# Optimization experiments

Hardware: AMD Instinct MI355X
Metric: run time of the kernel (lower is better)

The kernel has to match this reference:

```python
import jax, jax.numpy as jnp
import numpy as np

N = 100_000      # nodes
E = 1_600_000    # edges (before self-loops)
IN, OUT, HID = 64, 32, 64
BN_EPS = 1e-5

def _mlp(h, w1, b1, g, beta, w2, b2):
    # PyG MLP (num_layers=2, plain_last=True): Linear -> BatchNorm(train) -> ReLU -> Linear
    h = h @ w1 + b1
    mu = jnp.mean(h, axis=0)
    var = jnp.var(h, axis=0)
    h = (h - mu) * jax.lax.rsqrt(var + BN_EPS) * g + beta
    return jax.nn.relu(h) @ w2 + b2

def setup_inputs() -> dict:
    key = jax.random.key(0)
    ks = jax.random.split(key, 12)
    def rn(k, shape):
        fan_in = shape[0]
        return jax.random.normal(k, shape, jnp.float32) / np.sqrt(fan_in)
    x = jax.random.normal(ks[0], (N, IN), jnp.float32)
    pos = jax.random.normal(ks[1], (N, 3), jnp.float32)
    edge_index = jax.random.randint(ks[2], (2, E), 0, N, jnp.int64)
    return {
        "x": x, "pos": pos, "edge_index": edge_index,
        "w_lin": rn(ks[3], (IN, OUT)), "w_src": rn(ks[4], (IN, OUT)), "w_dst": rn(ks[5], (IN, OUT)),
        "pos_w1": rn(ks[6], (3, HID)), "pos_b1": jnp.zeros((HID,), jnp.float32),
        "pos_g": jnp.ones((HID,), jnp.float32), "pos_beta": jnp.zeros((HID,), jnp.float32),
        "pos_w2": rn(ks[7], (HID, OUT)), "pos_b2": jnp.zeros((OUT,), jnp.float32),
        "att_w1": rn(ks[8], (OUT, HID)), "att_b1": jnp.zeros((HID,), jnp.float32),
        "att_g": jnp.ones((HID,), jnp.float32), "att_beta": jnp.zeros((HID,), jnp.float32),
        "att_w2": rn(ks[9], (HID, OUT)), "att_b2": jnp.zeros((OUT,), jnp.float32),
    }

def reference(x, pos, edge_index, w_lin, w_src, w_dst,
              pos_w1, pos_b1, pos_g, pos_beta, pos_w2, pos_b2,
              att_w1, att_b1, att_g, att_beta, att_w2, att_b2):
    n = x.shape[0]
    # add self-loops (PointTransformerConv default add_self_loops=True)
    loops = jnp.arange(n, dtype=edge_index.dtype)
    src = jnp.concatenate([edge_index[0], loops])  # j (message source)
    dst = jnp.concatenate([edge_index[1], loops])  # i (message target)

    alpha_src = x @ w_src          # [N, OUT]
    alpha_dst = x @ w_dst          # [N, OUT]
    x_val = x @ w_lin              # [N, OUT]

    delta = _mlp(pos[dst] - pos[src], pos_w1, pos_b1, pos_g, pos_beta, pos_w2, pos_b2)  # [E', OUT]
    a = _mlp(alpha_dst[dst] - alpha_src[src] + delta, att_w1, att_b1, att_g, att_beta, att_w2, att_b2)

    # per-destination-node, per-channel softmax over incoming edges
    a_max = jax.ops.segment_max(a, dst, num_segments=n)           # [N, OUT]
    a = jnp.exp(a - a_max[dst])
    denom = jax.ops.segment_sum(a, dst, num_segments=n)           # [N, OUT]
    a = a / (denom[dst] + 1e-16)

    msg = a * (x_val[src] + delta)                                # [E', OUT]
    out = jax.ops.segment_sum(msg, dst, num_segments=n)           # [N, OUT]
    return out
```

## Files before the change

kernel.cpp:

```cpp
#include <hip/hip_runtime.h>

typedef unsigned int uint;
typedef unsigned short ushort;

#define BN_EPS 1e-5f

using bf16x8 = __attribute__((ext_vector_type(8))) short;
using f32x16 = __attribute__((ext_vector_type(16))) float;

union FragU { uint w[4]; bf16x8 v; };

__device__ __forceinline__ uint pk2(float lo, float hi) {
    uint r;
    asm("v_cvt_pk_bf16_f32 %0, %1, %2" : "=v"(r) : "v"(lo), "v"(hi));
    return r;
}
__device__ __forceinline__ float bfu_lo(uint u) { return __uint_as_float(u << 16); }
__device__ __forceinline__ float bfu_hi(uint u) { return __uint_as_float(u & 0xffff0000u); }

__device__ __forceinline__ float upk(const uint* p, int idx) {
    uint u = p[idx >> 1];
    return (idx & 1) ? bfu_hi(u) : bfu_lo(u);
}
__device__ __forceinline__ float upq(const uint2* gq, int r) {
// ... 237 lines not shown
{
    int c = threadIdx.x;
    if (c < 64) {
        float b   = bias ? bias[c] : 0.f;
        float m0  = stats[c] * inv_ep;
        float mu  = m0 + b;
        float eq  = stats[64+c] * inv_ep + 2.f*b*m0 + b*b;
        float var = fmaxf(eq - mu * mu, 0.f);
        float sc  = rsqrtf(var + BN_EPS) * g[c];
        bn[c]      = sc;
        bn[64+c]   = beta[c] - mu * sc;
    }
}

__global__ void k_fold1(const float* __restrict__ pw1, const float* __restrict__ pb1,
                        const float* __restrict__ bn1,
                        float* __restrict__ pw1f, float* __restrict__ pb1f)
{
    int i = threadIdx.x;
    if (i < 192) pw1f[i] = pw1[i] * bn1[i & 63];
    if (i < 64)  pb1f[i] = pb1[i] * bn1[i] + bn1[64 + i];
}

__global__ void k_fold2(const float* __restrict__ aw1, const float* __restrict__ ab1,
                        const float* __restrict__ bn2,
                        float* __restrict__ aw1f, float* __restrict__ ab1f)
{
    int i = blockIdx.x * 256 + threadIdx.x;
    if (i < 2048) aw1f[i] = aw1[i] * bn2[i & 63];
    if (i < 64)   ab1f[i] = ab1[i] * bn2[i] + bn2[64 + i];
}

template<bool SORTED>
__global__ __launch_bounds__(256, 3) void k_delta_stats(
    const int* __restrict__ ei, const int* __restrict__ srcs, const int* __restrict__ dsts,
    const float4* __restrict__ pos4,
    const uint* __restrict__ asx, const uint* __restrict__ aDb,
    const float* __restrict__ pw1f, const float* __restrict__ pb1f,
    const float* __restrict__ pw2, const float* __restrict__ pb2,
    const float* __restrict__ aw1,
    float* __restrict__ partD, int nE, int eTot)
{
    const int lane = threadIdx.x & 63;
    const int col  = lane & 31;
    const int h    = lane >> 5;

    __shared__ float redS[4][64], redQ[4][64];
    {
        int w = threadIdx.x >> 6, c = threadIdx.x & 63;
        redS[w][c] = 0.f; redQ[w][c] = 0.f;
    }

    bool quadOK;
    int q2[4];
    FragU fw_pw2[4];
    FragU fw_aw1[2][2];
    uint pb2p[8];
    {
        int rowv[16];
        get_rowmap(col, rowv);
        quadOK = true;
        #pragma unroll
        for (int g = 0; g < 4; g++)
            quadOK = quadOK && (rowv[4*g+1] == rowv[4*g]+1)
                            && (rowv[4*g+2] == rowv[4*g]+2)
                            && (rowv[4*g+3] == rowv[4*g]+3);
        #pragma unroll
        for (int g = 0; g < 4; g++) q2[g] = rowv[4*g] >> 2;
        #pragma unroll
        for (int kt = 0; kt < 4; kt++)
            #pragma unroll
            for (int jw = 0; jw < 4; jw++) {
                int m = 2*jw;
                int c0 = 16*kt + 8*(m>>2) + 4*h + (m&3);
                fw_pw2[kt].w[jw] = pk2(pw2[c0*32 + col], pw2[(c0+1)*32 + col]);
            }
        #pragma unroll
        for (int mt = 0; mt < 2; mt++)
            #pragma unroll
            for (int kt = 0; kt < 2; kt++)
                #pragma unroll
                for (int jw = 0; jw < 4; jw++) {
                    int u0 = rowv[8*kt + 2*jw], u1 = rowv[8*kt + 2*jw + 1];
                    fw_aw1[mt][kt].w[jw] = pk2(aw1[u0*64 + 32*mt + col],
                                               aw1[u1*64 + 32*mt + col]);
                }
        #pragma unroll
        for (int g = 0; g < 8; g++)
            pb2p[g] = pk2(pb2[rowv[2*g]], pb2[rowv[2*g+1]]);
    }

    float sA[32], qA[32];
    #pragma unroll
    for (int i = 0; i < 32; i++) { sA[i] = 0.f; qA[i] = 0.f; }

    const int nT = (eTot + 31) >> 5;
    const int gw = (blockIdx.x << 2) + (threadIdx.x >> 6);
    const int nW = gridDim.x << 2;

    if (quadOK) {
        for (int t = gw; t < nT; t += nW) {
            int e = t*32 + col;
            bool valid = e < eTot;
            int ec = valid ? e : eTot - 1;
            int src, dst;
            edge_sd<SORTED>(ec, ei, srcs, dsts, nE, src, dst);
            float4 ps = pos4[src], pd = pos4[dst];
            uint2 gs2[4], gd2[4];
            {
                const uint* rs = asx + (size_t)src*32;
                const uint* rd = aDb + (size_t)dst*16;
                #pragma unroll
                for (int g = 0; g < 4; g++) gs2[g] = *(const uint2*)(rs + 2*q2[g]);
                #pragma unroll
                for (int g = 0; g < 4; g++) gd2[g] = *(const uint2*)(rd + 2*q2[g]);
            }
            float p0 = pd.x - ps.x, p1 = pd.y - ps.y, p2 = pd.z - ps.z;

            FragU ft[4];
            #pragma unroll
            for (int kt = 0; kt < 4; kt++)
                #pragma unroll
                for (int mm = 0; mm < 2; mm++) {
                    int cb = 16*kt + 8*mm + 4*h;
                    float4 w0 = *(const float4*)(pw1f +       cb);
                    float4 w1 = *(const float4*)(pw1f + 64  + cb);
                    float4 w2 = *(const float4*)(pw1f + 128 + cb);
                    float4 bb = *(const float4*)(pb1f + cb);
                    float t0 = fmaxf(fmaf(p0,w0.x, fmaf(p1,w1.x, fmaf(p2,w2.x, bb.x))), 0.f);
                    float t1 = fmaxf(fmaf(p0,w0.y, fmaf(p1,w1.y, fmaf(p2,w2.y, bb.y))), 0.f);
                    float t2 = fmaxf(fmaf(p0,w0.z, fmaf(p1,w1.z, fmaf(p2,w2.z, bb.z))), 0.f);
                    float t3 = fmaxf(fmaf(p0,w0.w, fmaf(p1,w1.w, fmaf(p2,w2.w, bb.w))), 0.f);
                    ft[kt].w[2*mm+0] = pk2(t0, t1);
                    ft[kt].w[2*mm+1] = pk2(t2, t3);
                }
            f32x16 adl;
            #pragma unroll
            for (int r = 0; r < 16; r++) adl[r] = upk(pb2p, r);
            #pragma unroll
            for (int kt = 0; kt < 4; kt++)
                adl = __builtin_amdgcn_mfma_f32_32x32x16_bf16(fw_pw2[kt].v, ft[kt].v, adl, 0, 0, 0);

            FragU fu[2];
            #pragma unroll
            for (int kt = 0; kt < 2; kt++)
                #pragma unroll
                for (int jw = 0; jw < 4; jw++) {
                    int r0 = 8*kt + 2*jw;
                    fu[kt].w[jw] = pk2(adl[r0]   + upq(gd2, r0)   - upq(gs2, r0),
                                       adl[r0+1] + upq(gd2, r0+1) - upq(gs2, r0+1));
                }

            f32x16 ah0, ah1;
            #pragma unroll
            for (int r = 0; r < 16; r++) { ah0[r] = 0.f; ah1[r] = 0.f; }
            #pragma unroll
            for (int kt = 0; kt < 2; kt++) {
                ah0 = __builtin_amdgcn_mfma_f32_32x32x16_bf16(fw_aw1[0][kt].v, fu[kt].v, ah0, 0, 0, 0);
                ah1 = __builtin_amdgcn_mfma_f32_32x32x16_bf16(fw_aw1[1][kt].v, fu[kt].v, ah1, 0, 0, 0);
            }
            if (valid) {
                #pragma unroll
                for (int r = 0; r < 16; r++) {
                    sA[r]    += ah0[r];
                    qA[r]     = fmaf(ah0[r], ah0[r], qA[r]);
                    sA[16+r] += ah1[r];
                    qA[16+r]  = fmaf(ah1[r], ah1[r], qA[16+r]);
                }
            }
        }
    } else {
        int rowv[16];
        get_rowmap(col, rowv);
        for (int t = gw; t < nT; t += nW) {
            int e = t*32 + col;
            bool valid = e < eTot;
            int ec = valid ? e : eTot - 1;
            int src, dst;
            edge_sd<SORTED>(ec, ei, srcs, dsts, nE, src, dst);
            float4 pd = pos4[dst], ps = pos4[src];
            float p0 = pd.x - ps.x, p1 = pd.y - ps.y, p2 = pd.z - ps.z;
            FragU ft[4];
            #pragma unroll
            for (int kt = 0; kt < 4; kt++)
                #pragma unroll
                for (int mm = 0; mm < 2; mm++) {
                    int cb = 16*kt + 8*mm + 4*h;
                    float4 w0 = *(const float4*)(pw1f +       cb);
                    float4 w1 = *(const float4*)(pw1f + 64  + cb);
                    float4 w2 = *(const float4*)(pw1f + 128 + cb);
                    float4 bb = *(const float4*)(pb1f + cb);
                    float t0 = fmaxf(fmaf(p0,w0.x, fmaf(p1,w1.x, fmaf(p2,w2.x, bb.x))), 0.f);
                    float t1 = fmaxf(fmaf(p0,w0.y, fmaf(p1,w1.y, fmaf(p2,w2.y, bb.y))), 0.f);
                    float t2 = fmaxf(fmaf(p0,w0.z, fmaf(p1,w1.z, fmaf(p2,w2.z, bb.z))), 0.f);
                    float t3 = fmaxf(fmaf(p0,w0.w, fmaf(p1,w1.w, fmaf(p2,w2.w, bb.w))), 0.f);
                    ft[kt].w[2*mm+0] = pk2(t0, t1);
                    ft[kt].w[2*mm+1] = pk2(t2, t3);
                }
            f32x16 adl;
            #pragma unroll
            for (int r = 0; r < 16; r++) adl[r] = upk(pb2p, r);
            #pragma unroll
            for (int kt = 0; kt < 4; kt++)
                adl = __builtin_amdgcn_mfma_f32_32x32x16_bf16(fw_pw2[kt].v, ft[kt].v, adl, 0, 0, 0);
            const ushort* rs = (const ushort*)(asx + (size_t)src*32);
            const ushort* rd = (const ushort*)(aDb + (size_t)dst*16);
            FragU fu[2];
            #pragma unroll
            for (int kt = 0; kt < 2; kt++)
                #pragma unroll
                for (int jw = 0; jw < 4; jw++) {
                    int r0 = 8*kt + 2*jw;
                    float u0 = adl[r0]   + __uint_as_float(((uint)rd[rowv[r0]])   << 16)
                                         - __uint_as_float(((uint)rs[rowv[r0]])   << 16);
                    float u1 = adl[r0+1] + __uint_as_float(((uint)rd[rowv[r0+1]]) << 16)
                                         - __uint_as_float(((uint)rs[rowv[r0+1]]) << 16);
                    fu[kt].w[jw] = pk2(u0, u1);
                }
            f32x16 ah0, ah1;
            #pragma unroll
            for (int r = 0; r < 16; r++) { ah0[r] = 0.f; ah1[r] = 0.f; }
            #pragma unroll
            for (int kt = 0; kt < 2; kt++) {
                ah0 = __builtin_amdgcn_mfma_f32_32x32x16_bf16(fw_aw1[0][kt].v, fu[kt].v, ah0, 0, 0, 0);
                ah1 = __builtin_amdgcn_mfma_f32_32x32x16_bf16(fw_aw1[1][kt].v, fu[kt].v, ah1, 0, 0, 0);
            }
            if (valid) {
                #pragma unroll
                for (int r = 0; r < 16; r++) {
                    sA[r]    += ah0[r];
                    qA[r]     = fmaf(ah0[r], ah0[r], qA[r]);
                    sA[16+r] += ah1[r];
                    qA[16+r]  = fmaf(ah1[r], ah1[r], qA[16+r]);
                }
            }
        }
    }

    __syncthreads();
    {
        int rv[16];
        get_rowmap(col, rv);
        int w = threadIdx.x >> 6;
        #pragma unroll
        for (int idx = 0; idx < 32; idx++) {
            float vs = sA[idx], vq = qA[idx];
            for (int off = 16; off > 0; off >>= 1) {
                vs += __shfl_xor(vs, off, 64);
                vq += __shfl_xor(vq, off, 64);
            }
            if ((threadIdx.x & 31) == 0) {
                int mt = idx >> 4, r = idx & 15;
                int c = 32*mt + rv[r];
                redS[w][c] = vs;
                redQ[w][c] = vq;
            }
        }
    }
    __syncthreads();
    if (threadIdx.x < 64) {
        int c = threadIdx.x;
        float S = redS[0][c] + redS[1][c] + redS[2][c] + redS[3][c];
        float Q = redQ[0][c] + redQ[1][c] + redQ[2][c] + redQ[3][c];
        partD[(size_t)blockIdx.x*128 + c]      = S;
        partD[(size_t)blockIdx.x*128 + 64 + c] = Q;
    }
}

template<bool SORTED>
__global__ __launch_bounds__(256, 3) void k_att_agg(
    const int* __restrict__ ei, const int* __restrict__ srcs, const int* __restrict__ dsts,
    const float4* __restrict__ pos4,
    const uint* __restrict__ asx, const uint* __restrict__ aDb,
    const float* __restrict__ pw1f, const float* __restrict__ pb1f,
    const float* __restrict__ pw2, const float* __restrict__ pb2,
    const float* __restrict__ aw1f, const float* __restrict__ ab1f,
    const float* __restrict__ aw2, const float* __restrict__ ab2,
    float* __restrict__ denom, float* __restrict__ outp,
    int nE, int eTot)
{
    const int lane = threadIdx.x & 63;
    const int col  = lane & 31;
    const int h    = lane >> 5;

    bool quadOK;
    int q2[4];
    FragU fw_pw2[4], fw_aw2[4];
    FragU fw_aw1[2][2];
    uint pb2p[8], ab2p[8], ab1p[16];
    {
        int rowv[16];
        get_rowmap(col, rowv);
        quadOK = true;
        #pragma unroll
        for (int g = 0; g < 4; g++)
            quadOK = quadOK && (rowv[4*g+1] == rowv[4*g]+1)
                            && (rowv[4*g+2] == rowv[4*g]+2)
                            && (rowv[4*g+3] == rowv[4*g]+3);
        #pragma unroll
        for (int g = 0; g < 4; g++) q2[g] = rowv[4*g] >> 2;
        #pragma unroll
        for (int kt = 0; kt < 4; kt++)
            #pragma unroll
            for (int jw = 0; jw < 4; jw++) {
                int m = 2*jw;
                int c0 = 16*kt + 8*(m>>2) + 4*h + (m&3);
                fw_pw2[kt].w[jw] = pk2(pw2[c0*32 + col], pw2[(c0+1)*32 + col]);
                int o0 = 32*(kt>>1) + rowv[8*(kt&1) + m];
                int o1 = 32*(kt>>1) + rowv[8*(kt&1) + m + 1];
                fw_aw2[kt].w[jw] = pk2(aw2[o0*32 + col], aw2[o1*32 + col]);
            }
        #pragma unroll
        for (int mt = 0; mt < 2; mt++)
            #pragma unroll
            for (int kt = 0; kt < 2; kt++)
                #pragma unroll
                for (int jw = 0; jw < 4; jw++) {
                    int u0 = rowv[8*kt + 2*jw], u1 = rowv[8*kt + 2*jw + 1];
                    fw_aw1[mt][kt].w[jw] = pk2(aw1f[u0*64 + 32*mt + col],
                                               aw1f[u1*64 + 32*mt + col]);
                }
        #pragma unroll
        for (int g = 0; g < 8; g++) {
            pb2p[g] = pk2(pb2[rowv[2*g]], pb2[rowv[2*g+1]]);
            ab2p[g] = pk2(ab2[rowv[2*g]], ab2[rowv[2*g+1]]);
            ab1p[g]     = pk2(ab1f[rowv[2*g]],      ab1f[rowv[2*g+1]]);
            ab1p[8 + g] = pk2(ab1f[32 + rowv[2*g]], ab1f[32 + rowv[2*g+1]]);
        }
    }

    const int nT = (eTot + 31) >> 5;
    const int gw = (blockIdx.x << 2) + (threadIdx.x >> 6);
    const int nW = gridDim.x << 2;

    if (quadOK) {
        for (int t = gw; t < nT; t += nW) {
            int e = t*32 + col;
            bool valid = e < eTot;
            int ec = valid ? e : eTot - 1;
            int src, dst;
            edge_sd<SORTED>(ec, ei, srcs, dsts, nE, src, dst);
            float4 ps = pos4[src], pd = pos4[dst];
            uint2 gs2[4], gx2[4], gd2[4];
            {
                const uint* rs = asx + (size_t)src*32;
                #pragma unroll
                for (int g = 0; g < 4; g++) gs2[g] = *(const uint2*)(rs + 2*q2[g]);
                #pragma unroll
                for (int g = 0; g < 4; g++) gx2[g] = *(const uint2*)(rs + 16 + 2*q2[g]);
                const uint* rd = aDb + (size_t)dst*16;
                #pragma unroll
                for (int g = 0; g < 4; g++) gd2[g] = *(const uint2*)(rd + 2*q2[g]);
            }
            float p0 = pd.x - ps.x, p1 = pd.y - ps.y, p2 = pd.z - ps.z;

            FragU ft[4];
            #pragma unroll
            for (int kt = 0; kt < 4; kt++)
                #pragma unroll
                for (int mm = 0; mm < 2; mm++) {
                    int cb = 16*kt + 8*mm + 4*h;
                    float4 w0 = *(const float4*)(pw1f +       cb);
                    float4 w1 = *(const float4*)(pw1f + 64  + cb);
                    float4 w2 = *(const float4*)(pw1f + 128 + cb);
                    float4 bb = *(const float4*)(pb1f + cb);
                    float t0 = fmaxf(fmaf(p0,w0.x, fmaf(p1,w1.x, fmaf(p2,w2.x, bb.x))), 0.f);
                    float t1 = fmaxf(fmaf(p0,w0.y, fmaf(p1,w1.y, fmaf(p2,w2.y, bb.y))), 0.f);
                    float t2 = fmaxf(fmaf(p0,w0.z, fmaf(p1,w1.z, fmaf(p2,w2.z, bb.z))), 0.f);
                    float t3 = fmaxf(fmaf(p0,w0.w, fmaf(p1,w1.w, fmaf(p2,w2.w, bb.w))), 0.f);
                    ft[kt].w[2*mm+0] = pk2(t0, t1);
                    ft[kt].w[2*mm+1] = pk2(t2, t3);
                }
            f32x16 adl;
            #pragma unroll
            for (int r = 0; r < 16; r++) adl[r] = upk(pb2p, r);
            #pragma unroll
            for (int kt = 0; kt < 4; kt++)
                adl = __builtin_amdgcn_mfma_f32_32x32x16_bf16(fw_pw2[kt].v, ft[kt].v, adl, 0, 0, 0);

            FragU fu[2];
            #pragma unroll
            for (int kt = 0; kt < 2; kt++)
                #pragma unroll
                for (int jw = 0; jw < 4; jw++) {
                    int r0 = 8*kt + 2*jw;
                    fu[kt].w[jw] = pk2(adl[r0]   + upq(gd2, r0)   - upq(gs2, r0),
                                       adl[r0+1] + upq(gd2, r0+1) - upq(gs2, r0+1));
                }

            f32x16 ah0, ah1;
            #pragma unroll
            for (int r = 0; r < 16; r++) { ah0[r] = upk(ab1p, r); ah1[r] = upk(ab1p, 16 + r); }
            #pragma unroll
            for (int kt = 0; kt < 2; kt++) {
                ah0 = __builtin_amdgcn_mfma_f32_32x32x16_bf16(fw_aw1[0][kt].v, fu[kt].v, ah0, 0, 0, 0);
                ah1 = __builtin_amdgcn_mfma_f32_32x32x16_bf16(fw_aw1[1][kt].v, fu[kt].v, ah1, 0, 0, 0);
            }
            FragU fh[4];
            #pragma unroll
            for (int q = 0; q < 4; q++)
                #pragma unroll
                for (int jw = 0; jw < 4; jw++) {
                    int r0 = 8*(q&1) + 2*jw;
                    float x0 = (q < 2) ? ah0[r0]   : ah1[r0];
                    float x1 = (q < 2) ? ah0[r0+1] : ah1[r0+1];
                    fh[q].w[jw] = pk2(fmaxf(x0, 0.f), fmaxf(x1, 0.f));
                }
            f32x16 aa;
            #pragma unroll
            for (int r = 0; r < 16; r++) aa[r] = upk(ab2p, r);
            aa = __builtin_amdgcn_mfma_f32_32x32x16_bf16(fw_aw2[0].v, fh[0].v, aa, 0, 0, 0);
// ... 9 lines not shown
                bool eq2  = (__shfl_down(dst, 2, 32)  == dst) && (lw + 2  < 32);
                bool eq4  = (__shfl_down(dst, 4, 32)  == dst) && (lw + 4  < 32);
                bool eq8  = (__shfl_down(dst, 8, 32)  == dst) && (lw + 8  < 32);
                bool eq16 = (__shfl_down(dst, 16, 32) == dst) && (lw + 16 < 32);
                float* drow = denom + (size_t)dst * 32;
                float* orow = outp  + (size_t)dst * 32;
                #pragma unroll
                for (int r = 0; r < 16; r++) {
                    float ea = __expf(fminf(aa[r], 35.f));
                    float ev = valid ? ea : 0.f;
                    float mv = valid ? ea * (upq(gx2, r) + adl[r]) : 0.f;
                    { float a = __shfl_down(ev,1,32),  b = __shfl_down(mv,1,32);  if (eq1)  { ev += a; mv += b; } }
                    { float a = __shfl_down(ev,2,32),  b = __shfl_down(mv,2,32);  if (eq2)  { ev += a; mv += b; } }
                    { float a = __shfl_down(ev,4,32),  b = __shfl_down(mv,4,32);  if (eq4)  { ev += a; mv += b; } }
                    { float a = __shfl_down(ev,8,32),  b = __shfl_down(mv,8,32);  if (eq8)  { ev += a; mv += b; } }
                    { float a = __shfl_down(ev,16,32), b = __shfl_down(mv,16,32); if (eq16) { ev += a; mv += b; } }
                    if (isHead) {
                        int o = 4*q2[r>>2] + (r&3);
                        unsafeAtomicAdd(drow + o, ev);
                        unsafeAtomicAdd(orow + o, mv);
                    }
                }
            } else if (valid) {
                float* drow = denom + (size_t)dst * 32;
                float* orow = outp  + (size_t)dst * 32;
                #pragma unroll
                for (int r = 0; r < 16; r++) {
                    int o = 4*q2[r>>2] + (r&3);
                    float ea = __expf(fminf(aa[r], 35.f));
                    unsafeAtomicAdd(drow + o, ea);
                    unsafeAtomicAdd(orow + o, ea * (upq(gx2, r) + adl[r]));
                }
            }
        }
    } else {
        int rowv[16];
        get_rowmap(col, rowv);
        for (int t = gw; t < nT; t += nW) {
            int e = t*32 + col;
            bool valid = e < eTot;
            int ec = valid ? e : eTot - 1;
            int src, dst;
            edge_sd<SORTED>(ec, ei, srcs, dsts, nE, src, dst);
            float4 pd = pos4[dst], ps = pos4[src];
            float p0 = pd.x - ps.x, p1 = pd.y - ps.y, p2 = pd.z - ps.z;
            FragU ft[4];
            #pragma unroll
            for (int kt = 0; kt < 4; kt++)
                #pragma unroll
                for (int mm = 0; mm < 2; mm++) {
                    int cb = 16*kt + 8*mm + 4*h;
                    float4 w0 = *(const float4*)(pw1f +       cb);
                    float4 w1 = *(const float4*)(pw1f + 64  + cb);
                    float4 w2 = *(const float4*)(pw1f + 128 + cb);
                    float4 bb = *(const float4*)(pb1f + cb);
                    float t0 = fmaxf(fmaf(p0,w0.x, fmaf(p1,w1.x, fmaf(p2,w2.x, bb.x))), 0.f);
                    float t1 = fmaxf(fmaf(p0,w0.y, fmaf(p1,w1.y, fmaf(p2,w2.y, bb.y))), 0.f);
                    float t2 = fmaxf(fmaf(p0,w0.z, fmaf(p1,w1.z, fmaf(p2,w2.z, bb.z))), 0.f);
                    float t3 = fmaxf(fmaf(p0,w0.w, fmaf(p1,w1.w, fmaf(p2,w2.w, bb.w))), 0.f);
                    ft[kt].w[2*mm+0] = pk2(t0, t1);
                    ft[kt].w[2*mm+1] = pk2(t2, t3);
                }
            f32x16 adl;
            #pragma unroll
            for (int r = 0; r < 16; r++) adl[r] = upk(pb2p, r);
            #pragma unroll
            for (int kt = 0; kt < 4; kt++)
                adl = __builtin_amdgcn_mfma_f32_32x32x16_bf16(fw_pw2[kt].v, ft[kt].v, adl, 0, 0, 0);
            const ushort* rs = (const ushort*)(asx + (size_t)src*32);
            const ushort* rd = (const ushort*)(aDb + (size_t)dst*16);
            FragU fu[2];
            float xg[16];
            #pragma unroll
            for (int r = 0; r < 16; r++)
                xg[r] = __uint_as_float(((uint)rs[32 + rowv[r]]) << 16);
            #pragma unroll
            for (int kt = 0; kt < 2; kt++)
                #pragma unroll
                for (int jw = 0; jw < 4; jw++) {
                    int r0 = 8*kt + 2*jw;
                    float u0 = adl[r0]   + __uint_as_float(((uint)rd[rowv[r0]])   << 16)
                                         - __uint_as_float(((uint)rs[rowv[r0]])   << 16);
                    float u1 = adl[r0+1] + __uint_as_float(((uint)rd[rowv[r0+1]]) << 16)
                                         - __uint_as_float(((uint)rs[rowv[r0+1]]) << 16);
                    fu[kt].w[jw] = pk2(u0, u1);
                }
            f32x16 ah0, ah1;
            #pragma unroll
            for (int r = 0; r < 16; r++) { ah0[r] = upk(ab1p, r); ah1[r] = upk(ab1p, 16 + r); }
            #pragma unroll
            for (int kt = 0; kt < 2; kt++) {
                ah0 = __builtin_amdgcn_mfma_f32_32x32x16_bf16(fw_aw1[0][kt].v, fu[kt].v, ah0, 0, 0, 0);
                ah1 = __builtin_amdgcn_mfma_f32_32x32x16_bf16(fw_aw1[1][kt].v, fu[kt].v, ah1, 0, 0, 0);
            }
            FragU fh[4];
            #pragma unroll
            for (int q = 0; q < 4; q++)
                #pragma unroll
                for (int jw = 0; jw < 4; jw++) {
                    int r0 = 8*(q&1) + 2*jw;
                    float x0 = (q < 2) ? ah0[r0]   : ah1[r0];
                    float x1 = (q < 2) ? ah0[r0+1] : ah1[r0+1];
                    fh[q].w[jw] = pk2(fmaxf(x0, 0.f), fmaxf(x1, 0.f));
                }
            f32x16 aa;
            #pragma unroll
            for (int r = 0; r < 16; r++) aa[r] = upk(ab2p, r);
            aa = __builtin_amdgcn_mfma_f32_32x32x16_bf16(fw_aw2[0].v, fh[0].v, aa, 0, 0, 0);
            aa = __builtin_amdgcn_mfma_f32_32x32x16_bf16(fw_aw2[1].v, fh[1].v, aa, 0, 0, 0);
            aa = __builtin_amdgcn_mfma_f32_32x32x16_bf16(fw_aw2[2].v, fh[2].v, aa, 0, 0, 0);
            aa = __builtin_amdgcn_mfma_f32_32x32x16_bf16(fw_aw2[3].v, fh[3].v, aa, 0, 0, 0);
            if (SORTED) {
                int lw = lane & 31;
                int dprev = __shfl_up(dst, 1, 32);
                bool isHead = (lw == 0) || (dprev != dst);
                bool eq1  = (__shfl_down(dst, 1, 32)  == dst) && (lw + 1  < 32);
                bool eq2  = (__shfl_down(dst, 2, 32)  == dst) && (lw + 2  < 32);
                bool eq4  = (__shfl_down(dst, 4, 32)  == dst) && (lw + 4  < 32);
// ... 63 lines not shown
    const float* ab2   = (const float*)d_in[17];
    float* out = (float*)d_out;

    const int nNodes = in_sizes[0] / 64;
    const int nE     = in_sizes[2] / 2;
    const int eTot   = nE + nNodes;

    const int PMBLK = 1024;
    const int DBLK  = 2048;

    const size_t nF = (size_t)nNodes * 32;
    uint*   asx   = (uint*)d_ws;
    uint*   aDb   = asx + (size_t)nNodes*32;
    float*  pos4  = (float*)(aDb + (size_t)nNodes*16);
    float*  denom = pos4 + (size_t)nNodes*4;
    float*  stats = denom + nF;
    float*  bn1   = stats + 512;
    float*  bn2   = bn1 + 128;
    float*  pw1f  = bn2 + 128;
    float*  pb1f  = pw1f + 192;
    float*  aw1f  = pb1f + 64;
    float*  ab1f  = aw1f + 2048;
    float*  partM = ab1f + 64;
    float*  partD = partM + (size_t)PMBLK*9;
    float*  fend  = partD + (size_t)DBLK*128;

    int* cnt    = (int*)fend;
    int* cur    = cnt + nNodes;
    int* blkS   = cur + nNodes;
    int* blkOff = blkS + 256;
    int* srcs   = blkOff + 256;
    int* dsts   = srcs + eTot;

    size_t need_sorted = ((char*)(dsts + eTot)) - ((char*)d_ws);
    const bool sorted = ws_size >= need_sorted;

    const int nb = (nNodes + SCH - 1) / SCH;

    hipMemsetAsync(out,   0, nF * sizeof(float), stream);
    hipMemsetAsync(denom, 0, nF * sizeof(float), stream);

    k_node_lin<<<(nNodes + 255) / 256, 256, 0, stream>>>(
        x, w_src, w_dst, w_lin, asx, aDb, nNodes);
    k_pos4<<<(nNodes + 255) / 256, 256, 0, stream>>>(pos, (float4*)pos4, nNodes);

    k_pos_mom<<<PMBLK, 256, 0, stream>>>(ei, (const float4*)pos4, partM, nE);
    k_bn1_mom<<<1, 64, 0, stream>>>(partM, PMBLK, pw1, pb1, pg, pbeta, bn1,
                                    1.0f / (float)eTot);
    k_fold1<<<1, 256, 0, stream>>>(pw1, pb1, bn1, pw1f, pb1f);

    if (sorted) {
        hipMemsetAsync(cnt, 0, (size_t)nNodes * sizeof(int), stream);
        k_hist<<<(eTot + 255) / 256, 256, 0, stream>>>(ei, cnt, nE, eTot);
        k_scan1<<<nb, 256, 0, stream>>>(cnt, cur, blkS, nNodes);
        k_scan2<<<1, 256, 0, stream>>>(blkS, blkOff, nb);
        k_scan3<<<nb, 256, 0, stream>>>(cur, blkOff, nNodes);
        k_rank<<<(eTot + 255) / 256, 256, 0, stream>>>(ei, cur, srcs, dsts, nE, eTot);

        k_delta_stats<true><<<DBLK, 256, 0, stream>>>(
            ei, srcs, dsts, (const float4*)pos4, asx, aDb,
            pw1f, pb1f, pw2, pb2, aw1, partD, nE, eTot);
        k_red_stats<<<128, 256, 0, stream>>>(partD, stats + 128, DBLK);
        k_bn_fin<<<1, 64, 0, stream>>>(stats + 128, ag, abeta, ab1, bn2, 1.0f / (float)eTot);
        k_fold2<<<8, 256, 0, stream>>>(aw1, ab1, bn2, aw1f, ab1f);
        k_att_agg<true><<<DBLK, 256, 0, stream>>>(
            ei, srcs, dsts, (const float4*)pos4, asx, aDb,
            pw1f, pb1f, pw2, pb2, aw1f, ab1f, aw2, ab2, denom, out, nE, eTot);
// ... 14 lines not shown
```

Baseline: 930.4 us.

## Stage gathered source rows through swizzled LDS with cooperative 16-byte loads

In both edge kernels, each wave now cooperatively loads the 128-byte source-node rows (alpha_src and x_val) for its 32 edges. Eight lanes share each row and issue contiguous uint4 loads, which are written into a per-wave XOR-swizzled LDS buffer and read back later in the fragment layout the MFMA path needs. This replaces the scattered 8-byte per-lane gathers from global memory with coalesced row loads and moves the readback after the first MFMA to hide latency. It adds 16 KB of LDS per block, and the launch-bounds occupancy hint drops from 3 to 2 blocks. Wave-local LDS reuse across loop iterations depends on lockstep execution within the wave, since no barrier separates them.

Measured after the change: 852.7 us. 1.09x faster.

```diff
diff --git a/kernel.cpp b/kernel.cpp
--- a/kernel.cpp
+++ b/kernel.cpp
@@ -293,7 +293,7 @@
 }
 
 template<bool SORTED>
-__global__ __launch_bounds__(256, 3) void k_delta_stats(
+__global__ __launch_bounds__(256, 2) void k_delta_stats(
     const int* __restrict__ ei, const int* __restrict__ srcs, const int* __restrict__ dsts,
     const float4* __restrict__ pos4,
     const uint* __restrict__ asx, const uint* __restrict__ aDb,
@@ -305,8 +305,10 @@
     const int lane = threadIdx.x & 63;
     const int col  = lane & 31;
     const int h    = lane >> 5;
+    const int wid  = threadIdx.x >> 6;
 
     __shared__ float redS[4][64], redQ[4][64];
+    __shared__ uint sbuf[4][1024];
     {
         int w = threadIdx.x >> 6, c = threadIdx.x & 63;
         redS[w][c] = 0.f; redQ[w][c] = 0.f;
@@ -366,13 +368,18 @@
             int ec = valid ? e : eTot - 1;
             int src, dst;
             edge_sd<SORTED>(ec, ei, srcs, dsts, nE, src, dst);
+            #pragma unroll
+            for (int it = 0; it < 4; it++) {
+                int j  = it*8 + (lane >> 3);
+                int sj = __shfl(src, j, 64);
+                int w  = lane & 7;
+                uint4 v = *(const uint4*)(asx + (size_t)sj*32 + w*4);
+                *(uint4*)&sbuf[wid][j*32 + ((w ^ (j & 7)) << 2)] = v;
+            }
             float4 ps = pos4[src], pd = pos4[dst];
-            uint2 gs2[4], gd2[4];
+            uint2 gd2[4];
             {
-                const uint* rs = asx + (size_t)src*32;
                 const uint* rd = aDb + (size_t)dst*16;
-                #pragma unroll
-                for (int g = 0; g < 4; g++) gs2[g] = *(const uint2*)(rs + 2*q2[g]);
                 #pragma unroll
                 for (int g = 0; g < 4; g++) gd2[g] = *(const uint2*)(rd + 2*q2[g]);
             }
@@ -401,6 +408,13 @@
             #pragma unroll
             for (int kt = 0; kt < 4; kt++)
                 adl = __builtin_amdgcn_mfma_f32_32x32x16_bf16(fw_pw2[kt].v, ft[kt].v, adl, 0, 0, 0);
+
+            uint2 gs2[4];
+            #pragma unroll
+            for (int g = 0; g < 4; g++) {
+                int wq = q2[g] >> 1, hf = (q2[g] & 1) << 1;
+                gs2[g] = *(const uint2*)&sbuf[wid][col*32 + ((wq ^ (col & 7)) << 2) + hf];
+            }
 
             FragU fu[2];
             #pragma unroll
@@ -529,7 +543,7 @@
 }
 
 template<bool SORTED>
-__global__ __launch_bounds__(256, 3) void k_att_agg(
+__global__ __launch_bounds__(256, 2) void k_att_agg(
     const int* __restrict__ ei, const int* __restrict__ srcs, const int* __restrict__ dsts,
     const float4* __restrict__ pos4,
     const uint* __restrict__ asx, const uint* __restrict__ aDb,
@@ -543,6 +557,9 @@
     const int lane = threadIdx.x & 63;
     const int col  = lane & 31;
     const int h    = lane >> 5;
+    const int wid  = threadIdx.x >> 6;
+
+    __shared__ uint sbuf[4][1024];
 
     bool quadOK;
     int q2[4];
@@ -601,14 +618,17 @@
             int ec = valid ? e : eTot - 1;
             int src, dst;
             edge_sd<SORTED>(ec, ei, srcs, dsts, nE, src, dst);
+            #pragma unroll
+            for (int it = 0; it < 4; it++) {
+                int j  = it*8 + (lane >> 3);
+                int sj = __shfl(src, j, 64);
+                int w  = lane & 7;
+                uint4 v = *(const uint4*)(asx + (size_t)sj*32 + w*4);
+                *(uint4*)&sbuf[wid][j*32 + ((w ^ (j & 7)) << 2)] = v;
+            }
             float4 ps = pos4[src], pd = pos4[dst];
-            uint2 gs2[4], gx2[4], gd2[4];
+            uint2 gd2[4];
             {
-                const uint* rs = asx + (size_t)src*32;
-                #pragma unroll
-                for (int g = 0; g < 4; g++) gs2[g] = *(const uint2*)(rs + 2*q2[g]);
-                #pragma unroll
-                for (int g = 0; g < 4; g++) gx2[g] = *(const uint2*)(rs + 16 + 2*q2[g]);
                 const uint* rd = aDb + (size_t)dst*16;
                 #pragma unroll
                 for (int g = 0; g < 4; g++) gd2[g] = *(const uint2*)(rd + 2*q2[g]);
@@ -638,6 +658,14 @@
             #pragma unroll
             for (int kt = 0; kt < 4; kt++)
                 adl = __builtin_amdgcn_mfma_f32_32x32x16_bf16(fw_pw2[kt].v, ft[kt].v, adl, 0, 0, 0);
+
+            uint2 gs2[4], gx2[4];
+            #pragma unroll
+            for (int g = 0; g < 4; g++) {
+                int wq = q2[g] >> 1, hf = (q2[g] & 1) << 1;
+                gs2[g] = *(const uint2*)&sbuf[wid][col*32 + ((wq ^ (col & 7)) << 2) + hf];
+                gx2[g] = *(const uint2*)&sbuf[wid][col*32 + (((4 + wq) ^ (col & 7)) << 2) + hf];
+            }
 
             FragU fu[2];
             #pragma unroll
```

## Software-pipeline source-row gathers through LDS in attention aggregation kernel

Applied to the files above, without the earlier changes.

In k_att_agg the per-edge source feature rows (asx) are now fetched one tile ahead. Each wave issues coalesced 16-byte loads, with source indices broadcast by shuffle, and stages them in a swizzled shared-memory buffer, so gather latency overlaps the current tile's MFMA work and scattered 8-byte loads become wide loads. k_delta_stats merges its quad and non-quad loops into one loop with branches inside. Both kernels drop launch_bounds occupancy from 3 to 2 blocks per CU to leave room for the extra prefetch registers. The cost is more registers and LDS, lower occupancy, and an extra redundant prefetch on the last iteration.

Measured after the change: 812.4 us, median of 2. -12.7%, faster.

```diff
diff --git a/kernel.cpp b/kernel.cpp
--- a/kernel.cpp
+++ b/kernel.cpp
@@ -293,7 +293,7 @@
 }
 
 template<bool SORTED>
-__global__ __launch_bounds__(256, 3) void k_delta_stats(
+__global__ __launch_bounds__(256, 2) void k_delta_stats(
     const int* __restrict__ ei, const int* __restrict__ srcs, const int* __restrict__ dsts,
     const float4* __restrict__ pos4,
     const uint* __restrict__ asx, const uint* __restrict__ aDb,
@@ -317,8 +317,8 @@
     FragU fw_pw2[4];
     FragU fw_aw1[2][2];
     uint pb2p[8];
+    int rowv[16];
     {
-        int rowv[16];
         get_rowmap(col, rowv);
         quadOK = true;
         #pragma unroll
@@ -359,24 +359,242 @@
     const int gw = (blockIdx.x << 2) + (threadIdx.x >> 6);
     const int nW = gridDim.x << 2;
 
+    for (int t = gw; t < nT; t += nW) {
+        int e = t*32 + col;
+        bool valid = e < eTot;
+        int ec = valid ? e : eTot - 1;
+        int src, dst;
+        edge_sd<SORTED>(ec, ei, srcs, dsts, nE, src, dst);
+        float4 ps = pos4[src], pd = pos4[dst];
+        float p0 = pd.x - ps.x, p1 = pd.y - ps.y, p2 = pd.z - ps.z;
+
+        uint2 gs2[4], gd2[4];
+        float gSs[16], gDs[16];
+        if (quadOK) {
+            const uint* rs = asx + (size_t)src*32;
+            const uint* rd = aDb + (size_t)dst*16;
+            #pragma unroll
+            for (int g = 0; g < 4; g++) gs2[g] = *(const uint2*)(rs + 2*q2[g]);
+            #pragma unroll
+            for (int g = 0; g < 4; g++) gd2[g] = *(const uint2*)(rd + 2*q2[g]);
+        } else {
+            const ushort* rs = (const ushort*)(asx + (size_t)src*32);
+            const ushort* rd = (const ushort*)(aDb + (size_t)dst*16);
+            #pragma unroll
+            for (int r = 0; r < 16; r++) {
+                gSs[r] = __uint_as_float(((uint)rs[rowv[r]]) << 16);
+                gDs[r] = __uint_as_float(((uint)rd[rowv[r]]) << 16);
+            }
+        }
+
+        FragU ft[4];
+        #pragma unroll
+        for (int kt = 0; kt < 4; kt++)
+            #pragma unroll
+            for (int mm = 0; mm < 2; mm++) {
+                int cb = 16*kt + 8*mm + 4*h;
+                float4 w0 = *(const float4*)(pw1f +       cb);
+                float4 w1 = *(const float4*)(pw1f + 64  + cb);
+                float4 w2 = *(const float4*)(pw1f + 128 + cb);
+                float4 bb = *(const float4*)(pb1f + cb);
+                float t0 = fmaxf(fmaf(p0,w0.x, fmaf(p1,w1.x, fmaf(p2,w2.x, bb.x))), 0.f);
+                float t1 = fmaxf(fmaf(p0,w0.y, fmaf(p1,w1.y, fmaf(p2,w2.y, bb.y))), 0.f);
+                float t2 = fmaxf(fmaf(p0,w0.z, fmaf(p1,w1.z, fmaf(p2,w2.z, bb.z))), 0.f);
+                float t3 = fmaxf(fmaf(p0,w0.w, fmaf(p1,w1.w, fmaf(p2,w2.w, bb.w))), 0.f);
+                ft[kt].w[2*mm+0] = pk2(t0, t1);
+                ft[kt].w[2*mm+1] = pk2(t2, t3);
+            }
+        f32x16 adl;
+        #pragma unroll
+        for (int r = 0; r < 16; r++) adl[r] = upk(pb2p, r);
+        #pragma unroll
+        for (int kt = 0; kt < 4; kt++)
+            adl = __builtin_amdgcn_mfma_f32_32x32x16_bf16(fw_pw2[kt].v, ft[kt].v, adl, 0, 0, 0);
+
+        FragU fu[2];
+        if (quadOK) {
+            #pragma unroll
+            for (int kt = 0; kt < 2; kt++)
+                #pragma unroll
+                for (int jw = 0; jw < 4; jw++) {
+                    int r0 = 8*kt + 2*jw;
+                    fu[kt].w[jw] = pk2(adl[r0]   + upq(gd2, r0)   - upq(gs2, r0),
+                                       adl[r0+1] + upq(gd2, r0+1) - upq(gs2, r0+1));
+                }
+        } else {
+            #pragma unroll
+            for (int kt = 0; kt < 2; kt++)
+                #pragma unroll
+                for (int jw = 0; jw < 4; jw++) {
+                    int r0 = 8*kt + 2*jw;
+                    fu[kt].w[jw] = pk2(adl[r0]   + gDs[r0]   - gSs[r0],
+                                       adl[r0+1] + gDs[r0+1] - gSs[r0+1]);
+                }
+        }
+
+        f32x16 ah0, ah1;
+        #pragma unroll
+        for (int r = 0; r < 16; r++) { ah0[r] = 0.f; ah1[r] = 0.f; }
+        #pragma unroll
+        for (int kt = 0; kt < 2; kt++) {
+            ah0 = __builtin_amdgcn_mfma_f32_32x32x16_bf16(fw_aw1[0][kt].v, fu[kt].v, ah0, 0, 0, 0);
+            ah1 = __builtin_amdgcn_mfma_f32_32x32x16_bf16(fw_aw1[1][kt].v, fu[kt].v, ah1, 0, 0, 0);
+        }
+        if (valid) {
+            #pragma unroll
+            for (int r = 0; r < 16; r++) {
+                sA[r]    += ah0[r];
+                qA[r]     = fmaf(ah0[r], ah0[r], qA[r]);
+                sA[16+r] += ah1[r];
+                qA[16+r]  = fmaf(ah1[r], ah1[r], qA[16+r]);
+            }
+        }
+    }
+
+    __syncthreads();
+    {
+        int w = threadIdx.x >> 6;
+        #pragma unroll
+        for (int idx = 0; idx < 32; idx++) {
+            float vs = sA[idx], vq = qA[idx];
+            for (int off = 16; off > 0; off >>= 1) {
+                vs += __shfl_xor(vs, off, 64);
+                vq += __shfl_xor(vq, off, 64);
+            }
+            if ((threadIdx.x & 31) == 0) {
+                int mt = idx >> 4, r = idx & 15;
+                int c = 32*mt + rowv[r];
+                redS[w][c] = vs;
+                redQ[w][c] = vq;
+            }
+        }
+    }
+    __syncthreads();
+    if (threadIdx.x < 64) {
+        int c = threadIdx.x;
+        float S = redS[0][c] + redS[1][c] + redS[2][c] + redS[3][c];
+        float Q = redQ[0][c] + redQ[1][c] + redQ[2][c] + redQ[3][c];
+        partD[(size_t)blockIdx.x*128 + c]      = S;
+        partD[(size_t)blockIdx.x*128 + 64 + c] = Q;
+    }
+}
+
+template<bool SORTED>
+__global__ __launch_bounds__(256, 2) void k_att_agg(
+    const int* __restrict__ ei, const int* __restrict__ srcs, const int* __restrict__ dsts,
+    const float4* __restrict__ pos4,
+    const uint* __restrict__ asx, const uint* __restrict__ aDb,
+    const float* __restrict__ pw1f, const float* __restrict__ pb1f,
+    const float* __restrict__ pw2, const float* __restrict__ pb2,
+    const float* __restrict__ aw1f, const float* __restrict__ ab1f,
+    const float* __restrict__ aw2, const float* __restrict__ ab2,
+    float* __restrict__ denom, float* __restrict__ outp,
+    int nE, int eTot)
+{
+    const int lane = threadIdx.x & 63;
+    const int col  = lane & 31;
+    const int h    = lane >> 5;
+    const int wid  = threadIdx.x >> 6;
+
+    __shared__ uint sbuf[4][1024];
+
+    bool quadOK;
+    int q2[4];
+    int rowv[16];
+    FragU fw_pw2[4], fw_aw2[4];
+    FragU fw_aw1[2][2];
+    uint pb2p[8], ab2p[8], ab1p[16];
+    {
+        get_rowmap(col, rowv);
+        quadOK = true;
+        #pragma unroll
+        for (int g = 0; g < 4; g++)
+            quadOK = quadOK && (rowv[4*g+1] == rowv[4*g]+1)
+                            && (rowv[4*g+2] == rowv[4*g]+2)
+                            && (rowv[4*g+3] == rowv[4*g]+3);
+        #pragma unroll
+        for (int g = 0; g < 4; g++) q2[g] = rowv[4*g] >> 2;
+        #pragma unroll
+        for (int kt = 0; kt < 4; kt++)
+            #pragma unroll
+            for (int jw = 0; jw < 4; jw++) {
+                int m = 2*jw;
+                int c0 = 16*kt + 8*(m>>2) + 4*h + (m&3);
+                fw_pw2[kt].w[jw] = pk2(pw2[c0*32 + col], pw2[(c0+1)*32 + col]);
+                int o0 = 32*(kt>>1) + rowv[8*(kt&1) + m];
+                int o1 = 32*(kt>>1) + rowv[8*(kt&1) + m + 1];
+                fw_aw2[kt].w[jw] = pk2(aw2[o0*32 + col], aw2[o1*32 + col]);
+            }
+        #pragma unroll
+        for (int mt = 0; mt < 2; mt++)
+            #pragma unroll
+            for (int kt = 0; kt < 2; kt++)
+                #pragma unroll
+                for (int jw = 0; jw < 4; jw++) {
+                    int u0 = rowv[8*kt + 2*jw], u1 = rowv[8*kt + 2*jw + 1];
+                    fw_aw1[mt][kt].w[jw] = pk2(aw1f[u0*64 + 32*mt + col],
+                                               aw1f[u1*64 + 32*mt + col]);
+                }
+        #pragma unroll
+        for (int g = 0; g < 8; g++) {
+            pb2p[g] = pk2(pb2[rowv[2*g]], pb2[rowv[2*g+1]]);
+            ab2p[g] = pk2(ab2[rowv[2*g]], ab2[rowv[2*g+1]]);
+            ab1p[g]     = pk2(ab1f[rowv[2*g]],      ab1f[rowv[2*g+1]]);
+            ab1p[8 + g] = pk2(ab1f[32 + rowv[2*g]], ab1f[32 + rowv[2*g+1]]);
+        }
+    }
+
+    const int nT = (eTot + 31) >> 5;
+    const int gw = (blockIdx.x << 2) + (threadIdx.x >> 6);
+    const int nW = gridDim.x << 2;
+
     if (quadOK) {
-        for (int t = gw; t < nT; t += nW) {
+        int c_src, c_dst; float4 c_ps, c_pd; uint4 c_sv0, c_sv1, c_sv2, c_sv3;
+        int t = gw;
+        if (t < nT) {
             int e = t*32 + col;
-            bool valid = e < eTot;
-            int ec = valid ? e : eTot - 1;
-            int src, dst;
-            edge_sd<SORTED>(ec, ei, srcs, dsts, nE, src, dst);
-            float4 ps = pos4[src], pd = pos4[dst];
-            uint2 gs2[4], gd2[4];
+            int ec = (e < eTot) ? e : eTot - 1;
+            edge_sd<SORTED>(ec, ei, srcs, dsts, nE, c_src, c_dst);
+            c_ps = pos4[c_src]; c_pd = pos4[c_dst];
+            int w = lane & 7;
+            #define LDSTG(it, dstv) { int j = (it)*8 + (lane >> 3); int sj = __shfl(c_src, j, 64); \
+                dstv = *(const uint4*)(asx + (size_t)sj*32 + w*4); }
+            LDSTG(0, c_sv0) LDSTG(1, c_sv1) LDSTG(2, c_sv2) LDSTG(3, c_sv3)
+            #undef LDSTG
+        }
+        for (; t < nT; ) {
             {
-                const uint* rs = asx + (size_t)src*32;
+                int w = lane & 7;
+                #define STSTG(it, srcv) { int j = (it)*8 + (lane >> 3); \
+                    *(uint4*)&sbuf[wid][j*32 + ((w ^ (j & 7)) << 2)] = srcv; }
+                STSTG(0, c_sv0) STSTG(1, c_sv1) STSTG(2, c_sv2) STSTG(3, c_sv3)
+                #undef STSTG
+            }
+            int src = c_src, dst = c_dst;
+            bool valid = (t*32 + col) < eTot;
+            float p0 = c_pd.x - c_ps.x, p1 = c_pd.y - c_ps.y, p2 = c_pd.z - c_ps.z;
+
+            int tn = t + nW;
+            int tc = (tn < nT) ? tn : t;
+            int n_src, n_dst; float4 n_ps, n_pd; uint4 n_sv0, n_sv1, n_sv2, n_sv3;
+            {
+                int e2 = tc*32 + col;
+                int ec2 = (e2 < eTot) ? e2 : eTot - 1;
+                edge_sd<SORTED>(ec2, ei, srcs, dsts, nE, n_src, n_dst);
+                n_ps = pos4[n_src]; n_pd = pos4[n_dst];
+                int w = lane & 7;
+                #define LDSTG(it, dstv) { int j = (it)*8 + (lane >> 3); int sj = __shfl(n_src, j, 64); \
+                    dstv = *(const uint4*)(asx + (size_t)sj*32 + w*4); }
+                LDSTG(0, n_sv0) LDSTG(1, n_sv1) LDSTG(2, n_sv2) LDSTG(3, n_sv3)
+                #undef LDSTG
+            }
+
+            uint2 gd2[4];
+            {
                 const uint* rd = aDb + (size_t)dst*16;
                 #pragma unroll
-                for (int g = 0; g < 4; g++) gs2[g] = *(const uint2*)(rs + 2*q2[g]);
-                #pragma unroll
                 for (int g = 0; g < 4; g++) gd2[g] = *(const uint2*)(rd + 2*q2[g]);
             }
-            float p0 = pd.x - ps.x, p1 = pd.y - ps.y, p2 = pd.z - ps.z;
 
             FragU ft[4];
             #pragma unroll
@@ -402,242 +620,13 @@
             for (int kt = 0; kt < 4; kt++)
                 adl = __builtin_amdgcn_mfma_f32_32x32x16_bf16(fw_pw2[kt].v, ft[kt].v, adl, 0, 0, 0);
 
-            FragU fu[2];
-            #pragma unroll
-            for (int kt = 0; kt < 2; kt++)
-                #pragma unroll
-                for (int jw = 0; jw < 4; jw++) {
-                    int r0 = 8*kt + 2*jw;
-                    fu[kt].w[jw] = pk2(adl[r0]   + upq(gd2, r0)   - upq(gs2, r0),
-                                       adl[r0+1] + upq(gd2, r0+1) - upq(gs2, r0+1));
-                }
-
-            f32x16 ah0, ah1;
-            #pragma unroll
-            for (int r = 0; r < 16; r++) { ah0[r] = 0.f; ah1[r] = 0.f; }
-            #pragma unroll
-            for (int kt = 0; kt < 2; kt++) {
-                ah0 = __builtin_amdgcn_mfma_f32_32x32x16_bf16(fw_aw1[0][kt].v, fu[kt].v, ah0, 0, 0, 0);
-                ah1 = __builtin_amdgcn_mfma_f32_32x32x16_bf16(fw_aw1[1][kt].v, fu[kt].v, ah1, 0, 0, 0);
-            }
-            if (valid) {
-                #pragma unroll
-                for (int r = 0; r < 16; r++) {
-                    sA[r]    += ah0[r];
-                    qA[r]     = fmaf(ah0[r], ah0[r], qA[r]);
-                    sA[16+r] += ah1[r];
-                    qA[16+r]  = fmaf(ah1[r], ah1[r], qA[16+r]);
-                }
-            }
-        }
-    } else {
-        int rowv[16];
-        get_rowmap(col, rowv);
-        for (int t = gw; t < nT; t += nW) {
-            int e = t*32 + col;
-            bool valid = e < eTot;
-            int ec = valid ? e : eTot - 1;
-            int src, dst;
-            edge_sd<SORTED>(ec, ei, srcs, dsts, nE, src, dst);
-            float4 pd = pos4[dst], ps = pos4[src];
-            float p0 = pd.x - ps.x, p1 = pd.y - ps.y, p2 = pd.z - ps.z;
-            FragU ft[4];
-            #pragma unroll
-            for (int kt = 0; kt < 4; kt++)
-                #pragma unroll
-                for (int mm = 0; mm < 2; mm++) {
-                    int cb = 16*kt + 8*mm + 4*h;
-                    float4 w0 = *(const float4*)(pw1f +       cb);
-                    float4 w1 = *(const float4*)(pw1f + 64  + cb);
-                    float4 w2 = *(const float4*)(pw1f + 128 + cb);
-                    float4 bb = *(const float4*)(pb1f + cb);
-                    float t0 = fmaxf(fmaf(p0,w0.x, fmaf(p1,w1.x, fmaf(p2,w2.x, bb.x))), 0.f);
-                    float t1 = fmaxf(fmaf(p0,w0.y, fmaf(p1,w1.y, fmaf(p2,w2.y, bb.y))), 0.f);
-                    float t2 = fmaxf(fmaf(p0,w0.z, fmaf(p1,w1.z, fmaf(p2,w2.z, bb.z))), 0.f);
-                    float t3 = fmaxf(fmaf(p0,w0.w, fmaf(p1,w1.w, fmaf(p2,w2.w, bb.w))), 0.f);
-                    ft[kt].w[2*mm+0] = pk2(t0, t1);
-                    ft[kt].w[2*mm+1] = pk2(t2, t3);
-                }
-            f32x16 adl;
-            #pragma unroll
-            for (int r = 0; r < 16; r++) adl[r] = upk(pb2p, r);
-            #pragma unroll
-            for (int kt = 0; kt < 4; kt++)
-                adl = __builtin_amdgcn_mfma_f32_32x32x16_bf16(fw_pw2[kt].v, ft[kt].v, adl, 0, 0, 0);
-            const ushort* rs = (const ushort*)(asx + (size_t)src*32);
-            const ushort* rd = (const ushort*)(aDb + (size_t)dst*16);
-            FragU fu[2];
-            #pragma unroll
-            for (int kt = 0; kt < 2; kt++)
-                #pragma unroll
-                for (int jw = 0; jw < 4; jw++) {
-                    int r0 = 8*kt + 2*jw;
-                    float u0 = adl[r0]   + __uint_as_float(((uint)rd[rowv[r0]])   << 16)
-                                         - __uint_as_float(((uint)rs[rowv[r0]])   << 16);
-                    float u1 = adl[r0+1] + __uint_as_float(((uint)rd[rowv[r0+1]]) << 16)
-                                         - __uint_as_float(((uint)rs[rowv[r0+1]]) << 16);
-                    fu[kt].w[jw] = pk2(u0, u1);
-                }
-            f32x16 ah0, ah1;
-            #pragma unroll
-            for (int r = 0; r < 16; r++) { ah0[r] = 0.f; ah1[r] = 0.f; }
-            #pragma unroll
-            for (int kt = 0; kt < 2; kt++) {
-                ah0 = __builtin_amdgcn_mfma_f32_32x32x16_bf16(fw_aw1[0][kt].v, fu[kt].v, ah0, 0, 0, 0);
-                ah1 = __builtin_amdgcn_mfma_f32_32x32x16_bf16(fw_aw1[1][kt].v, fu[kt].v, ah1, 0, 0, 0);
-            }
-            if (valid) {
-                #pragma unroll
-                for (int r = 0; r < 16; r++) {
-                    sA[r]    += ah0[r];
-                    qA[r]     = fmaf(ah0[r], ah0[r], qA[r]);
-                    sA[16+r] += ah1[r];
-                    qA[16+r]  = fmaf(ah1[r], ah1[r], qA[16+r]);
-                }
-            }
-        }
-    }
-
-    __syncthreads();
-    {
-        int rv[16];
-        get_rowmap(col, rv);
-        int w = threadIdx.x >> 6;
-        #pragma unroll
-        for (int idx = 0; idx < 32; idx++) {
-            float vs = sA[idx], vq = qA[idx];
-            for (int off = 16; off > 0; off >>= 1) {
-                vs += __shfl_xor(vs, off, 64);
-                vq += __shfl_xor(vq, off, 64);
-            }
-            if ((threadIdx.x & 31) == 0) {
-                int mt = idx >> 4, r = idx & 15;
-                int c = 32*mt + rv[r];
-                redS[w][c] = vs;
-                redQ[w][c] = vq;
-            }
-        }
-    }
-    __syncthreads();
-    if (threadIdx.x < 64) {
-        int c = threadIdx.x;
-        float S = redS[0][c] + redS[1][c] + redS[2][c] + redS[3][c];
-        float Q = redQ[0][c] + redQ[1][c] + redQ[2][c] + redQ[3][c];
-        partD[(size_t)blockIdx.x*128 + c]      = S;
-        partD[(size_t)blockIdx.x*128 + 64 + c] = Q;
-    }
-}
-
-template<bool SORTED>
-__global__ __launch_bounds__(256, 3) void k_att_agg(
-    const int* __restrict__ ei, const int* __restrict__ srcs, const int* __restrict__ dsts,
-    const float4* __restrict__ pos4,
-    const uint* __restrict__ asx, const uint* __restrict__ aDb,
-    const float* __restrict__ pw1f, const float* __restrict__ pb1f,
-    const float* __restrict__ pw2, const float* __restrict__ pb2,
-    const float* __restrict__ aw1f, const float* __restrict__ ab1f,
-    const float* __restrict__ aw2, const float* __restrict__ ab2,
-    float* __restrict__ denom, float* __restrict__ outp,
-    int nE, int eTot)
-{
-    const int lane = threadIdx.x & 63;
-    const int col  = lane & 31;
-    const int h    = lane >> 5;
-
-    bool quadOK;
-    int q2[4];
-    FragU fw_pw2[4], fw_aw2[4];
-    FragU fw_aw1[2][2];
-    uint pb2p[8], ab2p[8], ab1p[16];
-    {
-        int rowv[16];
-        get_rowmap(col, rowv);
-        quadOK = true;
-        #pragma unroll
-        for (int g = 0; g < 4; g++)
-            quadOK = quadOK && (rowv[4*g+1] == rowv[4*g]+1)
-                            && (rowv[4*g+2] == rowv[4*g]+2)
-                            && (rowv[4*g+3] == rowv[4*g]+3);
-        #pragma unroll
-        for (int g = 0; g < 4; g++) q2[g] = rowv[4*g] >> 2;
-        #pragma unroll
-        for (int kt = 0; kt < 4; kt++)
-            #pragma unroll
-            for (int jw = 0; jw < 4; jw++) {
-                int m = 2*jw;
-                int c0 = 16*kt + 8*(m>>2) + 4*h + (m&3);
-                fw_pw2[kt].w[jw] = pk2(pw2[c0*32 + col], pw2[(c0+1)*32 + col]);
-                int o0 = 32*(kt>>1) + rowv[8*(kt&1) + m];
-                int o1 = 32*(kt>>1) + rowv[8*(kt&1) + m + 1];
-                fw_aw2[kt].w[jw] = pk2(aw2[o0*32 + col], aw2[o1*32 + col]);
-            }
-        #pragma unroll
-        for (int mt = 0; mt < 2; mt++)
-            #pragma unroll
-            for (int kt = 0; kt < 2; kt++)
-                #pragma unroll
-                for (int jw = 0; jw < 4; jw++) {
-                    int u0 = rowv[8*kt + 2*jw], u1 = rowv[8*kt + 2*jw + 1];
-                    fw_aw1[mt][kt].w[jw] = pk2(aw1f[u0*64 + 32*mt + col],
-                                               aw1f[u1*64 + 32*mt + col]);
-                }
-        #pragma unroll
-        for (int g = 0; g < 8; g++) {
-            pb2p[g] = pk2(pb2[rowv[2*g]], pb2[rowv[2*g+1]]);
-            ab2p[g] = pk2(ab2[rowv[2*g]], ab2[rowv[2*g+1]]);
-            ab1p[g]     = pk2(ab1f[rowv[2*g]],      ab1f[rowv[2*g+1]]);
-            ab1p[8 + g] = pk2(ab1f[32 + rowv[2*g]], ab1f[32 + rowv[2*g+1]]);
-        }
-    }
-
-    const int nT = (eTot + 31) >> 5;
-    const int gw = (blockIdx.x << 2) + (threadIdx.x >> 6);
-    const int nW = gridDim.x << 2;
-
-    if (quadOK) {
-        for (int t = gw; t < nT; t += nW) {
-            int e = t*32 + col;
-            bool valid = e < eTot;
-            int ec = valid ? e : eTot - 1;
-            int src, dst;
-            edge_sd<SORTED>(ec, ei, srcs, dsts, nE, src, dst);
-            float4 ps = pos4[src], pd = pos4[dst];
-            uint2 gs2[4], gx2[4], gd2[4];
-            {
-                const uint* rs = asx + (size_t)src*32;
-                #pragma unroll
-                for (int g = 0; g < 4; g++) gs2[g] = *(const uint2*)(rs + 2*q2[g]);
-                #pragma unroll
-                for (int g = 0; g < 4; g++) gx2[g] = *(const uint2*)(rs + 16 + 2*q2[g]);
-                const uint* rd = aDb + (size_t)dst*16;
-                #pragma unroll
-                for (int g = 0; g < 4; g++) gd2[g] = *(const uint2*)(rd + 2*q2[g]);
-            }
-            float p0 = pd.x - ps.x, p1 = pd.y - ps.y, p2 = pd.z - ps.z;
-
-            FragU ft[4];
-            #pragma unroll
-            for (int kt = 0; kt < 4; kt++)
-                #pragma unroll
-                for (int mm = 0; mm < 2; mm++) {
-                    int cb = 16*kt + 8*mm + 4*h;
-                    float4 w0 = *(const float4*)(pw1f +       cb);
-                    float4 w1 = *(const float4*)(pw1f + 64  + cb);
-                    float4 w2 = *(const float4*)(pw1f + 128 + cb);
-                    float4 bb = *(const float4*)(pb1f + cb);
-                    float t0 = fmaxf(fmaf(p0,w0.x, fmaf(p1,w1.x, fmaf(p2,w2.x, bb.x))), 0.f);
-                    float t1 = fmaxf(fmaf(p0,w0.y, fmaf(p1,w1.y, fmaf(p2,w2.y, bb.y))), 0.f);
-                    float t2 = fmaxf(fmaf(p0,w0.z, fmaf(p1,w1.z, fmaf(p2,w2.z, bb.z))), 0.f);
-                    float t3 = fmaxf(fmaf(p0,w0.w, fmaf(p1,w1.w, fmaf(p2,w2.w, bb.w))), 0.f);
-                    ft[kt].w[2*mm+0] = pk2(t0, t1);
-                    ft[kt].w[2*mm+1] = pk2(t2, t3);
-                }
-            f32x16 adl;
-            #pragma unroll
-            for (int r = 0; r < 16; r++) adl[r] = upk(pb2p, r);
-            #pragma unroll
-            for (int kt = 0; kt < 4; kt++)
-                adl = __builtin_amdgcn_mfma_f32_32x32x16_bf16(fw_pw2[kt].v, ft[kt].v, adl, 0, 0, 0);
+            uint2 gs2[4], gx2[4];
+            #pragma unroll
+            for (int g = 0; g < 4; g++) {
+                int wq = q2[g] >> 1, hf = (q2[g] & 1) << 1;
+                gs2[g] = *(const uint2*)&sbuf[wid][col*32 + ((wq ^ (col & 7)) << 2) + hf];
+                gx2[g] = *(const uint2*)&sbuf[wid][col*32 + (((4 + wq) ^ (col & 7)) << 2) + hf];
+            }
 
             FragU fu[2];
             #pragma unroll
@@ -713,10 +702,11 @@
                     unsafeAtomicAdd(orow + o, ea * (upq(gx2, r) + adl[r]));
                 }
             }
+            c_src = n_src; c_dst = n_dst; c_ps = n_ps; c_pd = n_pd;
+            c_sv0 = n_sv0; c_sv1 = n_sv1; c_sv2 = n_sv2; c_sv3 = n_sv3;
+            t = tn;
         }
     } else {
-        int rowv[16];
-        get_rowmap(col, rowv);
         for (int t = gw; t < nT; t += nW) {
             int e = t*32 + col;
             bool valid = e < eTot;
@@ -725,6 +715,15 @@
             edge_sd<SORTED>(ec, ei, srcs, dsts, nE, src, dst);
             float4 pd = pos4[dst], ps = pos4[src];
             float p0 = pd.x - ps.x, p1 = pd.y - ps.y, p2 = pd.z - ps.z;
+            const ushort* rs = (const ushort*)(asx + (size_t)src*32);
+            const ushort* rd = (const ushort*)(aDb + (size_t)dst*16);
+            float gSs[16], gDs[16], xg[16];
+            #pragma unroll
+            for (int r = 0; r < 16; r++) {
+                gSs[r] = __uint_as_float(((uint)rs[rowv[r]]) << 16);
+                gDs[r] = __uint_as_float(((uint)rd[rowv[r]]) << 16);
+                xg[r]  = __uint_as_float(((uint)rs[32 + rowv[r]]) << 16);
+            }
             FragU ft[4];
             #pragma unroll
             for (int kt = 0; kt < 4; kt++)
@@ -748,23 +747,14 @@
             #pragma unroll
             for (int kt = 0; kt < 4; kt++)
                 adl = __builtin_amdgcn_mfma_f32_32x32x16_bf16(fw_pw2[kt].v, ft[kt].v, adl, 0, 0, 0);
-            const ushort* rs = (const ushort*)(asx + (size_t)src*32);
-            const ushort* rd = (const ushort*)(aDb + (size_t)dst*16);
             FragU fu[2];
-            float xg[16];
-            #pragma unroll
-            for (int r = 0; r < 16; r++)
-                xg[r] = __uint_as_float(((uint)rs[32 + rowv[r]]) << 16);
             #pragma unroll
             for (int kt = 0; kt < 2; kt++)
                 #pragma unroll
                 for (int jw = 0; jw < 4; jw++) {
                     int r0 = 8*kt + 2*jw;
-                    float u0 = adl[r0]   + __uint_as_float(((uint)rd[rowv[r0]])   << 16)
-                                         - __uint_as_float(((uint)rs[rowv[r0]])   << 16);
-                    float u1 = adl[r0+1] + __uint_as_float(((uint)rd[rowv[r0+1]]) << 16)
-                                         - __uint_as_float(((uint)rs[rowv[r0+1]]) << 16);
-                    fu[kt].w[jw] = pk2(u0, u1);
+                    fu[kt].w[jw] = pk2(adl[r0]   + gDs[r0]   - gSs[r0],
+                                       adl[r0+1] + gDs[r0+1] - gSs[r0+1]);
                 }
             f32x16 ah0, ah1;
             #pragma unroll
@@ -894,7 +884,7 @@
     int* srcs   = blkOff + 256;
     int* dsts   = srcs + eTot;
 
-    size_t need_sorted = ((char*)(dsts + eTot)) - ((char*)d_ws);
+    size_t need_sorted = (char*)(dsts + eTot) - (char*)d_ws;
     const bool sorted = ws_size >= need_sorted;
 
     const int nb = (nNodes + SCH - 1) / SCH;
```
